# Optimization experiments

Hardware: AMD Instinct MI355X
Metric: run time of the kernel (lower is better)

## Reference

```python
import jax, jax.numpy as jnp
import numpy as np


def setup_inputs() -> dict:
    key = jax.random.key(0)
    ks = jax.random.split(key, 16)
    B, P, ENC = 128, 196, 2048          # batch, num pixels (14x14), encoder feature size
    E = D = A = 512                      # embed, decoder(hidden), attention sizes
    V, L = 10000, 52                     # vocab, max caption length
    s = 0.02
    rn = lambda k, shp: jax.random.normal(k, shp, jnp.float32) * s
    return {
        "features": jax.random.normal(ks[0], (B, P, ENC), jnp.float32),
        "captions": jax.random.randint(ks[1], (B, L), 0, V),
        "caption_lengths": jax.random.randint(ks[2], (B, 1), 2, L + 1),
        "emb": jax.random.uniform(ks[3], (V, E), jnp.float32, -0.1, 0.1),
        "W_enc_att": rn(ks[4], (ENC, A)), "b_enc_att": jnp.zeros((A,), jnp.float32),
        "W_dec_att": rn(ks[5], (D, A)),   "b_dec_att": jnp.zeros((A,), jnp.float32),
        "w_full": rn(ks[6], (A,)),        "b_full": jnp.zeros((), jnp.float32),
        "W_h0": rn(ks[7], (ENC, D)),      "b_h0": jnp.zeros((D,), jnp.float32),
        "W_c0": rn(ks[8], (ENC, D)),      "b_c0": jnp.zeros((D,), jnp.float32),
        "W_beta": rn(ks[9], (D, ENC)),    "b_beta": jnp.zeros((ENC,), jnp.float32),
        "W_ih": rn(ks[10], (E + ENC, 4 * D)), "b_ih": jnp.zeros((4 * D,), jnp.float32),
        "W_hh": rn(ks[11], (D, 4 * D)),       "b_hh": jnp.zeros((4 * D,), jnp.float32),
        "W_fc": jax.random.uniform(ks[12], (D, V), jnp.float32, -0.1, 0.1),
        "b_fc": jnp.zeros((V,), jnp.float32),
    }


def reference(features, captions, caption_lengths, emb,
              W_enc_att, b_enc_att, W_dec_att, b_dec_att, w_full, b_full,
              W_h0, b_h0, W_c0, b_c0, W_beta, b_beta,
              W_ih, b_ih, W_hh, b_hh, W_fc, b_fc):
    lens = caption_lengths[:, 0]
    order = jnp.argsort(-lens)                       # sort descending by length (stable)
    features = features[order]
    captions = captions[order]
    decode_lengths = lens[order] - 1                 # [B]
    T = captions.shape[1] - 1                        # static max decode length

    emb_seq = emb[captions[:, :T]]                   # [B,T,E]
    eo = features.mean(axis=1)                       # [B,ENC]
    h = eo @ W_h0 + b_h0                             # [B,D]
    c = eo @ W_c0 + b_c0
    enc_proj = features @ W_enc_att + b_enc_att      # [B,P,A] (precomputed, h-independent)

    def step(carry, xs):
        h, c = carry
        t, e_t = xs                                  # e_t: [B,E]
        mask = (decode_lengths > t)[:, None].astype(h.dtype)  # rows still decoding
        dec_proj = h @ W_dec_att + b_dec_att         # [B,A]
        scores = jax.nn.relu(enc_proj + dec_proj[:, None, :]) @ w_full + b_full  # [B,P]
        alpha = jax.nn.softmax(scores, axis=-1)      # [B,P]
        attw = jnp.einsum('bp,bpe->be', alpha, features)       # attention-weighted enc
        gate = jax.nn.sigmoid(h @ W_beta + b_beta)   # [B,ENC]
        x = jnp.concatenate([e_t, gate * attw], axis=1)        # [B,E+ENC]
        gates = x @ W_ih + b_ih + h @ W_hh + b_hh    # [B,4D], torch LSTMCell order i,f,g,o
        i, f, g, o = jnp.split(gates, 4, axis=1)
        c_new = jax.nn.sigmoid(f) * c + jax.nn.sigmoid(i) * jnp.tanh(g)
        h_new = jax.nn.sigmoid(o) * jnp.tanh(c_new)
        preds = h_new @ W_fc + b_fc                  # dropout is identity in eval
        h = mask * h_new + (1.0 - mask) * h          # freeze finished rows
        c = mask * c_new + (1.0 - mask) * c
        return (h, c), (preds * mask, alpha * mask)

    (_, _), (preds, alphas) = jax.lax.scan(
        step, (h, c), (jnp.arange(T), jnp.swapaxes(emb_seq, 0, 1)))
    predictions = jnp.swapaxes(preds, 0, 1)          # [B,T,V]
    alphas = jnp.swapaxes(alphas, 0, 1)              # [B,T,P]
    return predictions, captions, decode_lengths, alphas
```

## Files before the change

### kernel.cpp

```cpp
#include <hip/hip_runtime.h>
#include <math.h>

#define NB 128
#define NP 196
#define NENC 2048
#define NE 512
#define ND 512
#define NA 512
#define NV 10000
#define NVPAD 10112
#define NL 52
#define NT 51
#define KXH2 2560

typedef unsigned short u16;
typedef __attribute__((ext_vector_type(8))) short bf16x8;
typedef __attribute__((ext_vector_type(8))) unsigned short u16x8;
typedef __attribute__((ext_vector_type(4))) float f32x4;

#define MFMA16 __builtin_amdgcn_mfma_f32_16x16x32_bf16

__device__ __forceinline__ float sigmoidf_(float v) { return 1.0f / (1.0f + __expf(-v)); }
__device__ __forceinline__ float b2f(u16 u) { return __uint_as_float(((unsigned int)u) << 16); }
__device__ __forceinline__ u16 f2b(float f) {
  unsigned int u = __float_as_uint(f);
  unsigned int r = (u + 0x7FFFu + ((u >> 16) & 1u)) >> 16;
  return (u16)r;
}

__global__ void kSort(const int* __restrict__ cap_len, const int* __restrict__ captions,
                      int* __restrict__ order, int* __restrict__ nact,
                      int* __restrict__ dlen_sorted,
                      float* __restrict__ out_cap, float* __restrict__ out_dlen) {
  __shared__ int lens[NB];
  __shared__ int s_dl[NB];
  int tid = threadIdx.x;
  lens[tid] = cap_len[tid];
  __syncthreads();
  int li = lens[tid];
  int r = 0;
  for (int j = 0; j < NB; ++j) {
    int lj = lens[j];
    if (lj > li || (lj == li && j < tid)) r++;
  }
  order[r] = tid;
  s_dl[r] = li - 1;
  dlen_sorted[r] = li - 1;
  out_dlen[r] = (float)(li - 1);
  for (int l = 0; l < NL; ++l)
    out_cap[(size_t)r * NL + l] = (float)captions[(size_t)tid * NL + l];
  __syncthreads();
  if (tid < NT) {
    int cnt = 0;
    for (int j = 0; j < NB; ++j) cnt += (s_dl[j] > tid) ? 1 : 0;
    nact[tid] = cnt;
  }
}

__global__ void kAlphaZero(const int* __restrict__ nact, float* __restrict__ out_alph) {
  int t = blockIdx.x;
  int n0 = nact[t];
  int cnt = (NB - n0) * NP;
  for (int i = threadIdx.x; i < cnt; i += 256) {
    int b = n0 + i / NP;
    int p = i - (i / NP) * NP;
    out_alph[((size_t)b * NT + t) * NP + p] = 0.0f;
  }
}

__global__ __launch_bounds__(256) void kPredTail(const int* __restrict__ dlen_sorted,
                                                 float* __restrict__ out_pred) {
  int row = blockIdx.x;
  int d = dlen_sorted[row];
  int cnt = (NT - d) * NV;
  float* base = out_pred + (size_t)row * NT * NV + (size_t)d * NV;
  f32x4 z = {0.0f, 0.0f, 0.0f, 0.0f};
  int start = (blockIdx.y * 256 + threadIdx.x) * 4;
  int step = gridDim.y * 256 * 4;
  for (int i = start; i < cnt; i += step)
    *(f32x4*)&base[i] = z;
}

__global__ void kFeats(const float* __restrict__ features, const int* __restrict__ order,
                       u16* __restrict__ featsb) {
  int p = blockIdx.x, b = blockIdx.y, tid = threadIdx.x;
  const float* src = features + ((size_t)order[b] * NP + p) * NENC + tid * 8;
  u16* dst = featsb + ((size_t)b * NP + p) * NENC + tid * 8;
  float4 v0 = *(const float4*)src;
  float4 v1 = *(const float4*)(src + 4);
  u16x8 o;
  o[0] = f2b(v0.x); o[1] = f2b(v0.y); o[2] = f2b(v0.z); o[3] = f2b(v0.w);
  o[4] = f2b(v1.x); o[5] = f2b(v1.y); o[6] = f2b(v1.z); o[7] = f2b(v1.w);
  *(u16x8*)dst = o;
}

__device__ __forceinline__ float tfetch(int mode, int k, int n,
                                        const float* __restrict__ A,
                                        const float* __restrict__ B) {
  switch (mode) {
    case 0: return A[(size_t)k * NA + n];
    case 1: return (n < NA) ? A[(size_t)k * NA + n] : B[(size_t)k * NENC + (n - NA)];
    case 2: return A[(size_t)k * (4 * ND) + (n & 3) * ND + (n >> 2)];
    case 3: {
      int col = (n & 3) * ND + (n >> 2);
      return (k < NENC) ? A[(size_t)(NE + k) * (4 * ND) + col]
                        : B[(size_t)(k - NENC) * (4 * ND) + col];
    }
    case 4: return (n < NV) ? A[(size_t)k * NV + n] : 0.0f;
    default: return (n < NA) ? A[(size_t)k * ND + n] : B[(size_t)k * ND + (n - NA)];
  }
}

__global__ __launch_bounds__(256) void kTrans(const float* __restrict__ A,
                                              const float* __restrict__ B,
                                              u16* __restrict__ dst,
                                              int K, int N, int mode) {
  __shared__ u16 T[32][136];
  int n0 = blockIdx.x * 32, k0 = blockIdx.y * 128;
  int tid = threadIdx.x;
  int c = tid & 31, kr = tid >> 5;
#pragma unroll
  for (int pass = 0; pass < 16; ++pass) {
    int kl = pass * 8 + kr;
    T[c][kl] = f2b(tfetch(mode, k0 + kl, n0 + c, A, B));
  }
  __syncthreads();
  int row = tid >> 3, seg = tid & 7;
  u16x8 v0, v1;
#pragma unroll
  for (int j = 0; j < 8; ++j) { v0[j] = T[row][seg * 16 + j]; v1[j] = T[row][seg * 16 + 8 + j]; }
  *(u16x8*)&dst[(size_t)(n0 + row) * K + k0 + seg * 16] = v0;
  *(u16x8*)&dst[(size_t)(n0 + row) * K + k0 + seg * 16 + 8] = v1;
}

__global__ void kEmbA(const float* __restrict__ emb, const int* __restrict__ captions,
                      const int* __restrict__ order, u16* __restrict__ embA) {
  int t = blockIdx.x, b = blockIdx.y;
  int tok = captions[(size_t)order[b] * NL + t];
  int i = threadIdx.x * 2;
  float2 v = *(const float2*)(emb + (size_t)tok * NE + i);
  unsigned int w0 = (unsigned int)f2b(v.x) | ((unsigned int)f2b(v.y) << 16);
  *(unsigned int*)(embA + ((size_t)t * NB + b) * NE + i) = w0;
}

__global__ __launch_bounds__(256) void kEmbGemm(const u16* __restrict__ A,
                                                const u16* __restrict__ BT,
                                                u16* __restrict__ D) {
  int w = threadIdx.x >> 6, lane = threadIdx.x & 63;
  int lr = lane & 15, lg = lane >> 4;
  int mb = blockIdx.y * 128 + w * 32;
  int nb = blockIdx.x * 64;
  f32x4 acc[2][4] = {};
  const u16* a0 = A + (size_t)(mb + lr) * NE + lg * 8;
  const u16* a1 = a0 + 16 * NE;
  const u16* b0 = BT + (size_t)(nb + lr) * NE + lg * 8;
  for (int k0 = 0; k0 < NE; k0 += 32) {
    bf16x8 af0 = *(const bf16x8*)(a0 + k0);
    bf16x8 af1 = *(const bf16x8*)(a1 + k0);
#pragma unroll
    for (int nt = 0; nt < 4; ++nt) {
      bf16x8 bf = *(const bf16x8*)(b0 + (size_t)nt * 16 * NE + k0);
      acc[0][nt] = MFMA16(af0, bf, acc[0][nt], 0, 0, 0);
      acc[1][nt] = MFMA16(af1, bf, acc[1][nt], 0, 0, 0);
    }
  }
#pragma unroll
  for (int mt = 0; mt < 2; ++mt)
#pragma unroll
    for (int nt = 0; nt < 4; ++nt)
#pragma unroll
      for (int j = 0; j < 4; ++j) {
        int row = mb + mt * 16 + lg * 4 + j;
        int col = nb + nt * 16 + lr;
        D[(size_t)row * NENC + col] = f2b(acc[mt][nt][j]);
      }
}

__global__ void kEo(const u16* __restrict__ featsb, u16* __restrict__ eob) {
  int e = blockIdx.x * 256 + threadIdx.x;
  int b = blockIdx.y;
  const u16* f = featsb + (size_t)b * NP * NENC + e;
  float s = 0.0f;
  for (int p = 0; p < NP; ++p) s += b2f(f[(size_t)p * NENC]);
  eob[(size_t)b * NENC + e] = f2b(s * (1.0f / NP));
}

__global__ __launch_bounds__(64) void kHC0(const u16* __restrict__ eob,
                                           const u16* __restrict__ BT,
                                           const float* __restrict__ b_h0,
                                           const float* __restrict__ b_c0,
                                           u16* __restrict__ hb, u16* __restrict__ xh0,
                                           float* __restrict__ c) {
  int lane = threadIdx.x;
  int lr = lane & 15, lg = lane >> 4;
  int mb = blockIdx.y * 32, nb = blockIdx.x * 32;
  f32x4 acc[2][2] = {};
  const u16* a0 = eob + (size_t)(mb + lr) * NENC + lg * 8;
  const u16* a1 = a0 + 16 * NENC;
  const u16* b0 = BT + (size_t)(nb + lr) * NENC + lg * 8;
  const u16* b1 = b0 + 16 * NENC;
#pragma unroll 4
  for (int k0 = 0; k0 < NENC; k0 += 32) {
    bf16x8 af0 = *(const bf16x8*)(a0 + k0);
    bf16x8 af1 = *(const bf16x8*)(a1 + k0);
    bf16x8 bv0 = *(const bf16x8*)(b0 + k0);
    bf16x8 bv1 = *(const bf16x8*)(b1 + k0);
    acc[0][0] = MFMA16(af0, bv0, acc[0][0], 0, 0, 0);
    acc[1][0] = MFMA16(af1, bv0, acc[1][0], 0, 0, 0);
    acc[0][1] = MFMA16(af0, bv1, acc[0][1], 0, 0, 0);
    acc[1][1] = MFMA16(af1, bv1, acc[1][1], 0, 0, 0);
  }
#pragma unroll
  for (int mt = 0; mt < 2; ++mt)
#pragma unroll
    for (int nt = 0; nt < 2; ++nt)
#pragma unroll
      for (int j = 0; j < 4; ++j) {
        int row = mb + mt * 16 + lg * 4 + j;
        int n = nb + nt * 16 + lr;
        if (n < NA) {
          u16 hv = f2b(acc[mt][nt][j] + b_h0[n]);
          hb[(size_t)row * ND + n] = hv;
          xh0[(size_t)row * KXH2 + NENC + n] = hv;
        } else {
          c[(size_t)row * ND + (n - NA)] = acc[mt][nt][j] + b_c0[n - NA];
        }
      }
}

__global__ __launch_bounds__(256) void kEncProj(const u16* __restrict__ A,
                                                const u16* __restrict__ BT,
                                                const float* __restrict__ bias,
                                                u16* __restrict__ D) {
  __shared__ u16 As[2][128][72];
  int lin = ((int)blockIdx.x % 8) * 196 + (int)blockIdx.x / 8;
  int mt = lin >> 3, ntile = lin & 7;
  int mb = mt * 128, nb = ntile * 64;
  int tid = threadIdx.x;
  int w = tid >> 6, lane = tid & 63;
  int lr = lane & 15, lg = lane >> 4;

  int arow[4], akp[4];
  const u16* aptr[4];
#pragma unroll
  for (int i = 0; i < 4; ++i) {
    int idx = i * 256 + tid;
    arow[i] = idx >> 3;
    akp[i] = idx & 7;
    aptr[i] = A + (size_t)(mb + arow[i]) * NENC + akp[i] * 8;
  }
  u16x8 s0 = *(const u16x8*)(aptr[0]);
  u16x8 s1 = *(const u16x8*)(aptr[1]);
  u16x8 s2 = *(const u16x8*)(aptr[2]);
  u16x8 s3 = *(const u16x8*)(aptr[3]);
  *(u16x8*)&As[0][arow[0]][akp[0] * 8] = s0;
  *(u16x8*)&As[0][arow[1]][akp[1] * 8] = s1;
  *(u16x8*)&As[0][arow[2]][akp[2] * 8] = s2;
  *(u16x8*)&As[0][arow[3]][akp[3] * 8] = s3;

  f32x4 acc[2][4] = {};
  const u16* bbase = BT + (size_t)(nb + lr) * NENC + lg * 8;
  int cur = 0;
  int r0 = w * 32 + lr;

  for (int k0 = 0; k0 < NENC; k0 += 64) {
    __syncthreads();
    bool more = (k0 + 64 < NENC);
    if (more) {
      s0 = *(const u16x8*)(aptr[0] + k0 + 64);
      s1 = *(const u16x8*)(aptr[1] + k0 + 64);
      s2 = *(const u16x8*)(aptr[2] + k0 + 64);
      s3 = *(const u16x8*)(aptr[3] + k0 + 64);
    }
#pragma unroll
    for (int kh = 0; kh < 2; ++kh) {
      bf16x8 af0 = *(const bf16x8*)&As[cur][r0][kh * 32 + lg * 8];
      bf16x8 af1 = *(const bf16x8*)&As[cur][r0 + 16][kh * 32 + lg * 8];
#pragma unroll
      for (int nt = 0; nt < 4; ++nt) {
        bf16x8 bf = *(const bf16x8*)(bbase + (size_t)nt * 16 * NENC + k0 + kh * 32);
        acc[0][nt] = MFMA16(af0, bf, acc[0][nt], 0, 0, 0);
        acc[1][nt] = MFMA16(af1, bf, acc[1][nt], 0, 0, 0);
      }
    }
    if (more) {
      *(u16x8*)&As[cur ^ 1][arow[0]][akp[0] * 8] = s0;
      *(u16x8*)&As[cur ^ 1][arow[1]][akp[1] * 8] = s1;
      *(u16x8*)&As[cur ^ 1][arow[2]][akp[2] * 8] = s2;
      *(u16x8*)&As[cur ^ 1][arow[3]][akp[3] * 8] = s3;
    }
    cur ^= 1;
  }
  __syncthreads();
  u16* eps = (u16*)As;
#pragma unroll
  for (int m2 = 0; m2 < 2; ++m2)
#pragma unroll
    for (int nt = 0; nt < 4; ++nt)
#pragma unroll
      for (int j = 0; j < 4; ++j) {
        int rloc = w * 32 + m2 * 16 + lg * 4 + j;
        int col = nt * 16 + lr;
        eps[rloc * 72 + col] = f2b(acc[m2][nt][j] + bias[nb + col]);
      }
  __syncthreads();
#pragma unroll
  for (int i = 0; i < 4; ++i) {
    int idx = i * 256 + tid;
    int row = idx >> 3, seg = idx & 7;
    *(u16x8*)&D[(size_t)(mb + row) * NA + nb + seg * 8] = *(u16x8*)&eps[row * 72 + seg * 8];
  }
}

__global__ __launch_bounds__(64) void kDecGate(const u16* __restrict__ hb,
                                               const u16* __restrict__ BT,
                                               const float* __restrict__ b_dec,
                                               const float* __restrict__ b_beta,
                                               const int* __restrict__ nact, int t,
                                               float* __restrict__ dec_proj,
                                               float* __restrict__ gate_raw) {
  int nact_t = nact[t];
  int mb = blockIdx.y * 32;
  if (mb >= nact_t) return;
  int lane = threadIdx.x;
  int lr = lane & 15, lg = lane >> 4;
  int nb = blockIdx.x * 32;
  f32x4 acc[2][2] = {};
  const u16* a0 = hb + (size_t)(mb + lr) * ND + lg * 8;
  const u16* a1 = a0 + 16 * ND;
  const u16* b0 = BT + (size_t)(nb + lr) * ND + lg * 8;
  const u16* b1 = b0 + 16 * ND;
#pragma unroll 4
  for (int k0 = 0; k0 < ND; k0 += 32) {
    bf16x8 af0 = *(const bf16x8*)(a0 + k0);
    bf16x8 af1 = *(const bf16x8*)(a1 + k0);
    bf16x8 bv0 = *(const bf16x8*)(b0 + k0);
    bf16x8 bv1 = *(const bf16x8*)(b1 + k0);
    acc[0][0] = MFMA16(af0, bv0, acc[0][0], 0, 0, 0);
    acc[1][0] = MFMA16(af1, bv0, acc[1][0], 0, 0, 0);
    acc[0][1] = MFMA16(af0, bv1, acc[0][1], 0, 0, 0);
    acc[1][1] = MFMA16(af1, bv1, acc[1][1], 0, 0, 0);
  }
#pragma unroll
  for (int mt = 0; mt < 2; ++mt)
#pragma unroll
    for (int nt = 0; nt < 2; ++nt)
#pragma unroll
      for (int j = 0; j < 4; ++j) {
        int row = mb + mt * 16 + lg * 4 + j;
        int n = nb + nt * 16 + lr;
        if (n < NA)
          dec_proj[(size_t)row * NA + n] = acc[mt][nt][j] + b_dec[n];
        else
          gate_raw[(size_t)row * NENC + (n - NA)] = acc[mt][nt][j] + b_beta[n - NA];
      }
}

__global__ __launch_bounds__(512) void kSAX(const u16* __restrict__ featsb,
                                            const u16* __restrict__ encb,
                                            const float* __restrict__ dec_proj,
                                            const float* __restrict__ gate_raw,
                                            const float* __restrict__ w_full,
                                            const float* __restrict__ b_full,
                                            const int* __restrict__ nact, int t,
                                            u16* __restrict__ xh_w,
                                            float* __restrict__ out_alph) {
  int b = blockIdx.x, r = blockIdx.y, tid = threadIdx.x;
  if (b >= nact[t]) return;
  __shared__ float s_dp[NA], s_wf[NA], s_al[NP + 12], red[16];
  if (tid < NA) { s_dp[tid] = dec_proj[(size_t)b * NA + tid]; s_wf[tid] = w_full[tid]; }
  __syncthreads();
  int wave = tid >> 6, lane = tid & 63;
  float bf_ = b_full[0];
  for (int p = wave; p < NP; p += 8) {
    const u16* ep = encb + ((size_t)b * NP + p) * NA + lane * 8;
    u16x8 v = *(const u16x8*)ep;
    float acc = 0.0f;
#pragma unroll
    for (int j = 0; j < 8; ++j) {
      int a = lane * 8 + j;
      float vv = b2f(v[j]) + s_dp[a];
      acc += fmaxf(vv, 0.0f) * s_wf[a];
    }
#pragma unroll
    for (int off = 32; off; off >>= 1) acc += __shfl_down(acc, off);
    if (lane == 0) s_al[p] = acc + bf_;
  }
  __syncthreads();
  float mx = (tid < NP) ? s_al[tid] : -3.4e38f;
#pragma unroll
  for (int off = 32; off; off >>= 1) mx = fmaxf(mx, __shfl_down(mx, off));
  if (lane == 0) red[wave] = mx;
  __syncthreads();
  if (tid == 0) {
    float m = red[0];
    for (int i = 1; i < 8; ++i) m = fmaxf(m, red[i]);
    red[0] = m;
  }
  __syncthreads();
  float m2v = red[0];
  float e = 0.0f;
  if (tid < NP) { e = __expf(s_al[tid] - m2v); s_al[tid] = e; }
#pragma unroll
  for (int off = 32; off; off >>= 1) e += __shfl_down(e, off);
  if (lane == 0) red[8 + wave] = e;
  __syncthreads();
  if (tid == 0) {
    float s = 0.0f;
    for (int i = 0; i < 8; ++i) s += red[8 + i];
    red[8] = 1.0f / s;
  }
  __syncthreads();
  float inv = red[8];
  if (tid < NP) {
    float al = s_al[tid] * inv;
    s_al[tid] = al;
    if (r == 0) out_alph[((size_t)b * NT + t) * NP + tid] = al;
  }
  __syncthreads();
  int e0 = r * 1024 + tid * 2;
  float ac0 = 0.0f, ac1 = 0.0f;
  const u16* fb = featsb + (size_t)b * NP * NENC + e0;
#pragma unroll 4
  for (int p = 0; p < NP; ++p) {
    unsigned int v = *(const unsigned int*)(fb + (size_t)p * NENC);
    float al = s_al[p];
    ac0 += al * __uint_as_float(v << 16);
    ac1 += al * __uint_as_float(v & 0xffff0000u);
  }
  float g0 = sigmoidf_(gate_raw[(size_t)b * NENC + e0]);
  float g1 = sigmoidf_(gate_raw[(size_t)b * NENC + e0 + 1]);
  unsigned int wo = (unsigned int)f2b(ac0 * g0) | ((unsigned int)f2b(ac1 * g1) << 16);
  *(unsigned int*)(xh_w + (size_t)b * KXH2 + e0) = wo;
}

__global__ __launch_bounds__(1024) void kGatesLstm(const u16* __restrict__ xh_r,
                                                   const u16* __restrict__ WifgoT2,
                                                   const u16* __restrict__ embAll,
                                                   const float* __restrict__ b_ih,
                                                   const float* __restrict__ b_hh,
                                                   const int* __restrict__ nact, int t,
                                                   float* __restrict__ cst,
                                                   u16* __restrict__ hb,
                                                   u16* __restrict__ hnewAll_t,
                                                   u16* __restrict__ xh_w) {
  __shared__ float smem[8 * 32 * 33];
  int nact_t = nact[t];
  int tid = threadIdx.x;
  int w = tid >> 6, lane = tid & 63;
  int lr = lane & 15, lg = lane >> 4;
  int rt = blockIdx.x & 3, ct = blockIdx.x >> 2;
  int mb = rt * 32, nb = ct * 32;
  int kq = w >> 1, mh = w & 1;
  if (mb < nact_t) {
    f32x4 acc0 = {}, acc1 = {};
    const u16* pa = xh_r + (size_t)(mb + mh * 16 + lr) * KXH2 + kq * 320 + lg * 8;
    const u16* pb0 = WifgoT2 + (size_t)(nb + lr) * KXH2 + kq * 320 + lg * 8;
    const u16* pb1 = pb0 + (size_t)16 * KXH2;
#pragma unroll
    for (int k0 = 0; k0 < 320; k0 += 32) {
      bf16x8 af = *(const bf16x8*)(pa + k0);
      bf16x8 bv0 = *(const bf16x8*)(pb0 + k0);
      bf16x8 bv1 = *(const bf16x8*)(pb1 + k0);
      acc0 = MFMA16(af, bv0, acc0, 0, 0, 0);
      acc1 = MFMA16(af, bv1, acc1, 0, 0, 0);
    }
#pragma unroll
    for (int j = 0; j < 4; ++j) {
      int rr = kq * 32 + mh * 16 + lg * 4 + j;
      smem[rr * 33 + lr] = acc0[j];
      smem[rr * 33 + 16 + lr] = acc1[j];
    }
  }
  __syncthreads();
  if (tid < 256) {
    int row = tid >> 3, dl = tid & 7;
    int grow = mb + row;
    int d = ct * 8 + dl;
    size_t off = (size_t)grow * ND + d;
    if (grow < nact_t) {
      float g4[4];
#pragma unroll
      for (int g = 0; g < 4; ++g) {
        int col = dl * 4 + g;
        float s = 0.0f;
#pragma unroll
        for (int q = 0; q < 8; ++q) s += smem[(q * 32 + row) * 33 + col];
        s += b2f(embAll[((size_t)t * NB + grow) * NENC + nb + col]);
        g4[g] = s;
      }
      float gi = g4[0] + b_ih[d] + b_hh[d];
      float gf = g4[1] + b_ih[ND + d] + b_hh[ND + d];
      float gg = g4[2] + b_ih[2 * ND + d] + b_hh[2 * ND + d];
      float go = g4[3] + b_ih[3 * ND + d] + b_hh[3 * ND + d];
      float cn = sigmoidf_(gf) * cst[off] + sigmoidf_(gi) * tanhf(gg);
      float hn = sigmoidf_(go) * tanhf(cn);
      u16 hv = f2b(hn);
      cst[off] = cn;
      hb[off] = hv;
      hnewAll_t[off] = hv;
      xh_w[(size_t)grow * KXH2 + NENC + d] = hv;
    } else {
      xh_w[(size_t)grow * KXH2 + NENC + d] = hb[off];
    }
  }
}

__global__ __launch_bounds__(256) void kPredsAll6(const u16* __restrict__ hnewAll,
                                                  const u16* __restrict__ BT,
                                                  const float* __restrict__ b_fc,
                                                  const int* __restrict__ nact,
                                                  float* __restrict__ out_pred) {
  __shared__ float ts[128][68];
  int lin = ((int)blockIdx.x & 7) * 520 + ((int)blockIdx.x >> 3);
  if (lin >= 158 * 26) return;
  int nbi = lin / 26;
  int tp = lin - nbi * 26;
  int t0 = tp * 2;
  int t1 = t0 + 1;
  bool has1 = (t1 < NT);
  int nb = nbi * 64;
  int nact0 = nact[t0];
  int nact1 = has1 ? nact[t1] : 0;
  int w = threadIdx.x >> 6, lane = threadIdx.x & 63;
  int lr = lane & 15, lg = lane >> 4;
  int mb = w * 32;
  f32x4 acc0[2][4] = {};
  f32x4 acc1[2][4] = {};
  bool do0 = (mb < nact0);
  bool do1 = has1 && (mb < nact1);
  if (do0) {
    const u16* a0 = hnewAll + (size_t)t0 * NB * ND + (size_t)(mb + lr) * ND + lg * 8;
    const u16* a1 = a0 + 16 * ND;
    const u16* a0b = a0 + (size_t)NB * ND;
    const u16* a1b = a1 + (size_t)NB * ND;
    const u16* b0 = BT + (size_t)(nb + lr) * ND + lg * 8;
    for (int k0 = 0; k0 < ND; k0 += 32) {
      bf16x8 bf0 = *(const bf16x8*)(b0 + k0);
      bf16x8 bf1 = *(const bf16x8*)(b0 + (size_t)16 * ND + k0);
      bf16x8 bf2 = *(const bf16x8*)(b0 + (size_t)32 * ND + k0);
      bf16x8 bf3 = *(const bf16x8*)(b0 + (size_t)48 * ND + k0);
      bf16x8 af0 = *(const bf16x8*)(a0 + k0);
      bf16x8 af1 = *(const bf16x8*)(a1 + k0);
      acc0[0][0] = MFMA16(af0, bf0, acc0[0][0], 0, 0, 0);
      acc0[1][0] = MFMA16(af1, bf0, acc0[1][0], 0, 0, 0);
      acc0[0][1] = MFMA16(af0, bf1, acc0[0][1], 0, 0, 0);
      acc0[1][1] = MFMA16(af1, bf1, acc0[1][1], 0, 0, 0);
      acc0[0][2] = MFMA16(af0, bf2, acc0[0][2], 0, 0, 0);
      acc0[1][2] = MFMA16(af1, bf2, acc0[1][2], 0, 0, 0);
      acc0[0][3] = MFMA16(af0, bf3, acc0[0][3], 0, 0, 0);
      acc0[1][3] = MFMA16(af1, bf3, acc0[1][3], 0, 0, 0);
      if (do1) {
        bf16x8 ag0 = *(const bf16x8*)(a0b + k0);
        bf16x8 ag1 = *(const bf16x8*)(a1b + k0);
        acc1[0][0] = MFMA16(ag0, bf0, acc1[0][0], 0, 0, 0);
        acc1[1][0] = MFMA16(ag1, bf0, acc1[1][0], 0, 0, 0);
        acc1[0][1] = MFMA16(ag0, bf1, acc1[0][1], 0, 0, 0);
        acc1[1][1] = MFMA16(ag1, bf1, acc1[1][1], 0, 0, 0);
        acc1[0][2] = MFMA16(ag0, bf2, acc1[0][2], 0, 0, 0);
        acc1[1][2] = MFMA16(ag1, bf2, acc1[1][2], 0, 0, 0);
        acc1[0][3] = MFMA16(ag0, bf3, acc1[0][3], 0, 0, 0);
        acc1[1][3] = MFMA16(ag1, bf3, acc1[1][3], 0, 0, 0);
      }
    }
  }
  int tid = threadIdx.x;
#pragma unroll
  for (int mt = 0; mt < 2; ++mt)
#pragma unroll
    for (int nt = 0; nt < 4; ++nt)
#pragma unroll
      for (int j = 0; j < 4; ++j) {
        int row = mb + mt * 16 + lg * 4 + j;
        int gn = nb + nt * 16 + lr;
        float bias = (gn < NV) ? b_fc[gn] : 0.0f;
        ts[row][nt * 16 + lr] = acc0[mt][nt][j] + bias;
      }
  __syncthreads();
#pragma unroll
  for (int i = 0; i < 8; ++i) {
    int idx = i * 256 + tid;
    int row = idx >> 4;
    int c4 = (idx & 15) * 4;
    int gn = nb + c4;
    if (row < nact0 && gn < NV) {
      f32x4 v = *(const f32x4*)&ts[row][c4];
      *(f32x4*)&out_pred[((size_t)row * NT + t0) * NV + gn] = v;
    }
  }
  if (!has1) return;
  __syncthreads();
#pragma unroll
  for (int mt = 0; mt < 2; ++mt)
#pragma unroll
    for (int nt = 0; nt < 4; ++nt)
#pragma unroll
      for (int j = 0; j < 4; ++j) {
        int row = mb + mt * 16 + lg * 4 + j;
        int gn = nb + nt * 16 + lr;
        float bias = (gn < NV) ? b_fc[gn] : 0.0f;
        ts[row][nt * 16 + lr] = acc1[mt][nt][j] + bias;
      }
  __syncthreads();
#pragma unroll
  for (int i = 0; i < 8; ++i) {
    int idx = i * 256 + tid;
    int row = idx >> 4;
    int c4 = (idx & 15) * 4;
    int gn = nb + c4;
    if (row < nact1 && gn < NV) {
      f32x4 v = *(const f32x4*)&ts[row][c4];
      *(f32x4*)&out_pred[((size_t)row * NT + t1) * NV + gn] = v;
    }
  }
}

extern "C" void kernel_launch(void* const* d_in, const int* in_sizes, int n_in,
                              void* d_out, int out_size, void* d_ws, size_t ws_size,
                              hipStream_t stream) {
  (void)in_sizes; (void)n_in; (void)out_size; (void)ws_size;
  const float* features  = (const float*)d_in[0];
  const int*   captions  = (const int*)d_in[1];
  const int*   cap_len   = (const int*)d_in[2];
  const float* emb       = (const float*)d_in[3];
  const float* W_enc_att = (const float*)d_in[4];
  const float* b_enc_att = (const float*)d_in[5];
  const float* W_dec_att = (const float*)d_in[6];
  const float* b_dec_att = (const float*)d_in[7];
  const float* w_full    = (const float*)d_in[8];
  const float* b_full    = (const float*)d_in[9];
  const float* W_h0      = (const float*)d_in[10];
  const float* b_h0      = (const float*)d_in[11];
  const float* W_c0      = (const float*)d_in[12];
  const float* b_c0      = (const float*)d_in[13];
  const float* W_beta    = (const float*)d_in[14];
  const float* b_beta    = (const float*)d_in[15];
  const float* W_ih      = (const float*)d_in[16];
  const float* b_ih      = (const float*)d_in[17];
  const float* W_hh      = (const float*)d_in[18];
  const float* b_hh      = (const float*)d_in[19];
  const float* W_fc      = (const float*)d_in[20];
  const float* b_fc      = (const float*)d_in[21];

  float* out      = (float*)d_out;
  float* out_pred = out;
  float* out_cap  = out_pred + (size_t)NB * NT * NV;
  float* out_dlen = out_cap + (size_t)NB * NL;
  float* out_alph = out_dlen + NB;

  char* p = (char*)d_ws;
  auto alloc = [&](size_t nbytes) { void* r = (void*)p; p += (nbytes + 255) & ~(size_t)255; return r; };
  int*   order    = (int*)alloc(NB * 4);
  int*   nact     = (int*)alloc(NT * 4);
  int*   dlen_s   = (int*)alloc(NB * 4);
  u16*   eob      = (u16*)alloc((size_t)NB * NENC * 2);
  float* c        = (float*)alloc((size_t)NB * ND * 4);
  u16*   hb       = (u16*)alloc((size_t)NB * ND * 2);
  u16*   xh0      = (u16*)alloc((size_t)NB * KXH2 * 2);
  u16*   xh1      = (u16*)alloc((size_t)NB * KXH2 * 2);
  u16*   hnewAll  = (u16*)alloc((size_t)NT * NB * ND * 2);
  float* dec_proj = (float*)alloc((size_t)NB * NA * 4);
  float* gate_raw = (float*)alloc((size_t)NB * NENC * 4);
  u16*   featsb   = (u16*)alloc((size_t)NB * NP * NENC * 2);
  u16*   encb     = (u16*)alloc((size_t)NB * NP * NA * 2);
  u16*   WencT    = (u16*)alloc((size_t)NA * NENC * 2);
  u16*   WdgT     = (u16*)alloc((size_t)(NA + NENC) * ND * 2);
  u16*   WihTopT  = (u16*)alloc((size_t)NENC * NE * 2);
  u16*   WifgoT2  = (u16*)alloc((size_t)NENC * KXH2 * 2);
  u16*   WfcT     = (u16*)alloc((size_t)NVPAD * ND * 2);
  u16*   WhcT     = (u16*)alloc((size_t)1024 * NENC * 2);
  u16*   embA     = (u16*)alloc((size_t)NT * NB * NE * 2);
  u16*   embAll   = (u16*)alloc((size_t)NT * NB * NENC * 2);

  kSort<<<1, NB, 0, stream>>>(cap_len, captions, order, nact, dlen_s, out_cap, out_dlen);
  kAlphaZero<<<NT, 256, 0, stream>>>(nact, out_alph);
  kPredTail<<<dim3(NB, 16), 256, 0, stream>>>(dlen_s, out_pred);
  kFeats<<<dim3(NP, NB), 256, 0, stream>>>(features, order, featsb);
  kTrans<<<dim3(512 / 32, 2048 / 128), 256, 0, stream>>>(W_enc_att, nullptr, WencT, 2048, 512, 0);
  kTrans<<<dim3(2560 / 32, 512 / 128), 256, 0, stream>>>(W_dec_att, W_beta, WdgT, 512, 2560, 1);
  kTrans<<<dim3(2048 / 32, 512 / 128), 256, 0, stream>>>(W_ih, nullptr, WihTopT, 512, 2048, 2);
  kTrans<<<dim3(2048 / 32, 2560 / 128), 256, 0, stream>>>(W_ih, W_hh, WifgoT2, 2560, 2048, 3);
  kTrans<<<dim3(NVPAD / 32, 512 / 128), 256, 0, stream>>>(W_fc, nullptr, WfcT, 512, NVPAD, 4);
  kTrans<<<dim3(1024 / 32, 2048 / 128), 256, 0, stream>>>(W_h0, W_c0, WhcT, 2048, 1024, 5);
  kEmbA<<<dim3(NT, NB), 256, 0, stream>>>(emb, captions, order, embA);
  kEmbGemm<<<dim3(NENC / 64, NT), 256, 0, stream>>>(embA, WihTopT, embAll);
  kEo<<<dim3(NENC / 256, NB), 256, 0, stream>>>(featsb, eob);
  kHC0<<<dim3(1024 / 32, NB / 32), 64, 0, stream>>>(eob, WhcT, b_h0, b_c0, hb, xh0, c);
  kEncProj<<<1568, 256, 0, stream>>>(featsb, WencT, b_enc_att, encb);

  for (int t = 0; t < NT; ++t) {
    u16* xh_r = (t & 1) ? xh1 : xh0;
    u16* xh_w = (t & 1) ? xh0 : xh1;
    kDecGate<<<dim3((NA + NENC) / 32, 4), 64, 0, stream>>>(hb, WdgT, b_dec_att, b_beta,
                                                           nact, t, dec_proj, gate_raw);
    kSAX<<<dim3(NB, 2), 512, 0, stream>>>(featsb, encb, dec_proj, gate_raw, w_full, b_full,
                                          nact, t, xh_r, out_alph);
    kGatesLstm<<<256, 1024, 0, stream>>>(xh_r, WifgoT2, embAll, b_ih, b_hh, nact, t,
                                         c, hb, hnewAll + (size_t)t * NB * ND, xh_w);
  }
  kPredsAll6<<<4160, 256, 0, stream>>>(hnewAll, WfcT, b_fc, nact, out_pred);
}
```

Before: 3.766 ms.

## Use fp8 feature copy for attention-weighted sum and remap block indices

Adds an fp8 (e4m3) copy of the sorted features, written alongside the bf16 copy in kFeats. kSAX now reads these fp8 bytes for the per-step attention-weighted reduction, with one block per batch row handling four encoder channels per thread. This halves the bytes streamed every timestep and drops the duplicated softmax done by the second block. kDecGate and kGatesLstm also remap their block indices, plausibly so that blocks sharing weight columns land on different XCDs. Storing features in fp8 reduces the precision of the attention context, which may hurt accuracy against the fp32 reference.

```diff
diff --git a/kernel.cpp b/kernel.cpp
--- a/kernel.cpp
+++ b/kernel.cpp
@@ -14,6 +14,7 @@
 #define KXH2 2560
 
 typedef unsigned short u16;
+typedef unsigned char u8;
 typedef __attribute__((ext_vector_type(8))) short bf16x8;
 typedef __attribute__((ext_vector_type(8))) unsigned short u16x8;
 typedef __attribute__((ext_vector_type(4))) float f32x4;
@@ -26,6 +27,38 @@
   unsigned int u = __float_as_uint(f);
   unsigned int r = (u + 0x7FFFu + ((u >> 16) & 1u)) >> 16;
   return (u16)r;
+}
+
+template <int SEL>
+__device__ __forceinline__ float fp8tof(unsigned int data) {
+#if __has_builtin(__builtin_amdgcn_cvt_f32_fp8)
+  return __builtin_amdgcn_cvt_f32_fp8(data, SEL);
+#else
+  unsigned int b = (data >> (SEL * 8)) & 0xFFu;
+  unsigned int s = (b & 0x80u) << 24;
+  unsigned int em = b & 0x7Fu;
+  float mag;
+  if ((em >> 3) == 0) mag = (float)em * 0.001953125f;
+  else mag = __uint_as_float((((em >> 3) + 120) << 23) | ((em & 7u) << 20));
+  return __uint_as_float(s | __float_as_uint(mag));
+#endif
+}
+__device__ __forceinline__ u8 ftofp8(float f) {
+  unsigned int u = __float_as_uint(f);
+  unsigned int s = (u >> 24) & 0x80u;
+  float af = fabsf(f);
+  if (af >= 448.0f) return (u8)(s | 0x7Eu);
+  if (af < 0.015625f) {
+    int m = (int)(af * 512.0f + 0.5f);
+    if (m >= 8) return (u8)(s | 0x08u);
+    return (u8)(s | (unsigned int)m);
+  }
+  int e = (int)((u >> 23) & 0xFF) - 127;
+  unsigned int m3 = (u >> 20) & 7u;
+  unsigned int rest = u & 0xFFFFFu;
+  if (rest > 0x80000u || (rest == 0x80000u && (m3 & 1u))) { m3++; if (m3 == 8u) { m3 = 0u; e++; } }
+  if (e > 8) return (u8)(s | 0x7Eu);
+  return (u8)(s | ((unsigned int)(e + 7) << 3) | m3);
 }
 
 __global__ void kSort(const int* __restrict__ cap_len, const int* __restrict__ captions,
@@ -82,16 +115,21 @@
 }
 
 __global__ void kFeats(const float* __restrict__ features, const int* __restrict__ order,
-                       u16* __restrict__ featsb) {
+                       u16* __restrict__ featsb, u8* __restrict__ featsb8) {
   int p = blockIdx.x, b = blockIdx.y, tid = threadIdx.x;
   const float* src = features + ((size_t)order[b] * NP + p) * NENC + tid * 8;
-  u16* dst = featsb + ((size_t)b * NP + p) * NENC + tid * 8;
   float4 v0 = *(const float4*)src;
   float4 v1 = *(const float4*)(src + 4);
   u16x8 o;
   o[0] = f2b(v0.x); o[1] = f2b(v0.y); o[2] = f2b(v0.z); o[3] = f2b(v0.w);
   o[4] = f2b(v1.x); o[5] = f2b(v1.y); o[6] = f2b(v1.z); o[7] = f2b(v1.w);
-  *(u16x8*)dst = o;
+  *(u16x8*)(featsb + ((size_t)b * NP + p) * NENC + tid * 8) = o;
+  uint2 q;
+  q.x = (unsigned int)ftofp8(v0.x) | ((unsigned int)ftofp8(v0.y) << 8) |
+        ((unsigned int)ftofp8(v0.z) << 16) | ((unsigned int)ftofp8(v0.w) << 24);
+  q.y = (unsigned int)ftofp8(v1.x) | ((unsigned int)ftofp8(v1.y) << 8) |
+        ((unsigned int)ftofp8(v1.z) << 16) | ((unsigned int)ftofp8(v1.w) << 24);
+  *(uint2*)(featsb8 + ((size_t)b * NP + p) * NENC + tid * 8) = q;
 }
 
 __device__ __forceinline__ float tfetch(int mode, int k, int n,
@@ -320,11 +358,12 @@
                                                float* __restrict__ dec_proj,
                                                float* __restrict__ gate_raw) {
   int nact_t = nact[t];
-  int mb = blockIdx.y * 32;
+  int lin = ((int)blockIdx.x % 8) * 40 + (int)blockIdx.x / 8;
+  int mb = (lin & 3) * 32;
   if (mb >= nact_t) return;
+  int nb = (lin >> 2) * 32;
   int lane = threadIdx.x;
   int lr = lane & 15, lg = lane >> 4;
-  int nb = blockIdx.x * 32;
   f32x4 acc[2][2] = {};
   const u16* a0 = hb + (size_t)(mb + lr) * ND + lg * 8;
   const u16* a1 = a0 + 16 * ND;
@@ -356,7 +395,7 @@
       }
 }
 
-__global__ __launch_bounds__(512) void kSAX(const u16* __restrict__ featsb,
+__global__ __launch_bounds__(512) void kSAX(const u8* __restrict__ featsb8,
                                             const u16* __restrict__ encb,
                                             const float* __restrict__ dec_proj,
                                             const float* __restrict__ gate_raw,
@@ -365,7 +404,7 @@
                                             const int* __restrict__ nact, int t,
                                             u16* __restrict__ xh_w,
                                             float* __restrict__ out_alph) {
-  int b = blockIdx.x, r = blockIdx.y, tid = threadIdx.x;
+  int b = blockIdx.x, tid = threadIdx.x;
   if (b >= nact[t]) return;
   __shared__ float s_dp[NA], s_wf[NA], s_al[NP + 12], red[16];
   if (tid < NA) { s_dp[tid] = dec_proj[(size_t)b * NA + tid]; s_wf[tid] = w_full[tid]; }
@@ -415,23 +454,28 @@
   if (tid < NP) {
     float al = s_al[tid] * inv;
     s_al[tid] = al;
-    if (r == 0) out_alph[((size_t)b * NT + t) * NP + tid] = al;
-  }
-  __syncthreads();
-  int e0 = r * 1024 + tid * 2;
-  float ac0 = 0.0f, ac1 = 0.0f;
-  const u16* fb = featsb + (size_t)b * NP * NENC + e0;
-#pragma unroll 4
+    out_alph[((size_t)b * NT + t) * NP + tid] = al;
+  }
+  __syncthreads();
+  int e0 = tid * 4;
+  float ac0 = 0.0f, ac1 = 0.0f, ac2 = 0.0f, ac3 = 0.0f;
+  const u8* fb = featsb8 + (size_t)b * NP * NENC + e0;
+#pragma unroll 2
   for (int p = 0; p < NP; ++p) {
     unsigned int v = *(const unsigned int*)(fb + (size_t)p * NENC);
     float al = s_al[p];
-    ac0 += al * __uint_as_float(v << 16);
-    ac1 += al * __uint_as_float(v & 0xffff0000u);
-  }
-  float g0 = sigmoidf_(gate_raw[(size_t)b * NENC + e0]);
-  float g1 = sigmoidf_(gate_raw[(size_t)b * NENC + e0 + 1]);
-  unsigned int wo = (unsigned int)f2b(ac0 * g0) | ((unsigned int)f2b(ac1 * g1) << 16);
-  *(unsigned int*)(xh_w + (size_t)b * KXH2 + e0) = wo;
+    ac0 += al * fp8tof<0>(v);
+    ac1 += al * fp8tof<1>(v);
+    ac2 += al * fp8tof<2>(v);
+    ac3 += al * fp8tof<3>(v);
+  }
+  const float* gr = gate_raw + (size_t)b * NENC + e0;
+  unsigned int lo = (unsigned int)f2b(ac0 * sigmoidf_(gr[0])) |
+                    ((unsigned int)f2b(ac1 * sigmoidf_(gr[1])) << 16);
+  unsigned int hi = (unsigned int)f2b(ac2 * sigmoidf_(gr[2])) |
+                    ((unsigned int)f2b(ac3 * sigmoidf_(gr[3])) << 16);
+  uint2 o; o.x = lo; o.y = hi;
+  *(uint2*)(xh_w + (size_t)b * KXH2 + e0) = o;
 }
 
 __global__ __launch_bounds__(1024) void kGatesLstm(const u16* __restrict__ xh_r,
@@ -449,7 +493,8 @@
   int tid = threadIdx.x;
   int w = tid >> 6, lane = tid & 63;
   int lr = lane & 15, lg = lane >> 4;
-  int rt = blockIdx.x & 3, ct = blockIdx.x >> 2;
+  int lin = ((int)blockIdx.x % 8) * 32 + (int)blockIdx.x / 8;
+  int rt = lin & 3, ct = lin >> 2;
   int mb = rt * 32, nb = ct * 32;
   int kq = w >> 1, mh = w & 1;
   if (mb < nact_t) {
@@ -527,9 +572,8 @@
   int mb = w * 32;
   f32x4 acc0[2][4] = {};
   f32x4 acc1[2][4] = {};
-  bool do0 = (mb < nact0);
   bool do1 = has1 && (mb < nact1);
-  if (do0) {
+  if (mb < nact0) {
     const u16* a0 = hnewAll + (size_t)t0 * NB * ND + (size_t)(mb + lr) * ND + lg * 8;
     const u16* a1 = a0 + 16 * ND;
     const u16* a0b = a0 + (size_t)NB * ND;
@@ -662,6 +706,7 @@
   float* dec_proj = (float*)alloc((size_t)NB * NA * 4);
   float* gate_raw = (float*)alloc((size_t)NB * NENC * 4);
   u16*   featsb   = (u16*)alloc((size_t)NB * NP * NENC * 2);
+  u8*    featsb8  = (u8*)alloc((size_t)NB * NP * NENC);
   u16*   encb     = (u16*)alloc((size_t)NB * NP * NA * 2);
   u16*   WencT    = (u16*)alloc((size_t)NA * NENC * 2);
   u16*   WdgT     = (u16*)alloc((size_t)(NA + NENC) * ND * 2);
@@ -675,7 +720,7 @@
   kSort<<<1, NB, 0, stream>>>(cap_len, captions, order, nact, dlen_s, out_cap, out_dlen);
   kAlphaZero<<<NT, 256, 0, stream>>>(nact, out_alph);
   kPredTail<<<dim3(NB, 16), 256, 0, stream>>>(dlen_s, out_pred);
-  kFeats<<<dim3(NP, NB), 256, 0, stream>>>(features, order, featsb);
+  kFeats<<<dim3(NP, NB), 256, 0, stream>>>(features, order, featsb, featsb8);
   kTrans<<<dim3(512 / 32, 2048 / 128), 256, 0, stream>>>(W_enc_att, nullptr, WencT, 2048, 512, 0);
   kTrans<<<dim3(2560 / 32, 512 / 128), 256, 0, stream>>>(W_dec_att, W_beta, WdgT, 512, 2560, 1);
   kTrans<<<dim3(2048 / 32, 512 / 128), 256, 0, stream>>>(W_ih, nullptr, WihTopT, 512, 2048, 2);
@@ -691,10 +736,9 @@
   for (int t = 0; t < NT; ++t) {
     u16* xh_r = (t & 1) ? xh1 : xh0;
     u16* xh_w = (t & 1) ? xh0 : xh1;
-    kDecGate<<<dim3((NA + NENC) / 32, 4), 64, 0, stream>>>(hb, WdgT, b_dec_att, b_beta,
-                                                           nact, t, dec_proj, gate_raw);
-    kSAX<<<dim3(NB, 2), 512, 0, stream>>>(featsb, encb, dec_proj, gate_raw, w_full, b_full,
-                                          nact, t, xh_r, out_alph);
+    kDecGate<<<320, 64, 0, stream>>>(hb, WdgT, b_dec_att, b_beta, nact, t, dec_proj, gate_raw);
+    kSAX<<<NB, 512, 0, stream>>>(featsb8, encb, dec_proj, gate_raw, w_full, b_full,
+                                 nact, t, xh_r, out_alph);
     kGatesLstm<<<256, 1024, 0, stream>>>(xh_r, WifgoT2, embAll, b_ih, b_hh, nact, t,
                                          c, hb, hnewAll + (size_t)t * NB * ND, xh_w);
   }
```

New measurement: 4.418 ms. 17.3% more time.
